# Optimization experiments

Measured on AMD Instinct MI355X. Metric: run time of the kernel, lower is better.

The kernel has to match this reference:

```python
import jax, jax.numpy as jnp
import numpy as np

T_MAX = 20  # max_seq_length


def setup_inputs() -> dict:
    key = jax.random.key(0)
    ks = jax.random.split(key, 24)
    B, H, A, V, Tc = 64, 512, 512, 50257, 19
    s = 0.02
    inp = {}
    inp["features"] = jax.random.normal(ks[0], (B, H), jnp.float32)
    inp["captions"] = jax.random.randint(ks[1], (B, Tc), 0, V)
    lens = jax.random.randint(ks[2], (B, 1), 1, T_MAX + 1)
    inp["lengths"] = -jnp.sort(-lens, axis=0)  # descending so sort_ind is identity
    inp["embed_table"] = jax.random.uniform(ks[3], (V, H), jnp.float32, -0.1, 0.1)
    # LSTM cell (PyTorch layout): input = [emb; attended] -> 2H
    inp["W_ih"] = jax.random.normal(ks[4], (4 * H, 2 * H), jnp.float32) * s
    inp["W_hh"] = jax.random.normal(ks[5], (4 * H, H), jnp.float32) * s
    inp["b_ih"] = jnp.zeros((4 * H,), jnp.float32)
    inp["b_hh"] = jnp.zeros((4 * H,), jnp.float32)
    # attention
    inp["W_enc"] = jax.random.normal(ks[6], (H, A), jnp.float32) * s
    inp["b_enc"] = jnp.zeros((A,), jnp.float32)
    inp["W_dec"] = jax.random.normal(ks[7], (H, A), jnp.float32) * s
    inp["b_dec"] = jnp.zeros((A,), jnp.float32)
    inp["W_full"] = jax.random.normal(ks[8], (A, 1), jnp.float32) * s
    inp["b_full"] = jnp.zeros((1,), jnp.float32)
    # init_h / init_c / f_beta / fc
    inp["W_hinit"] = jax.random.normal(ks[9], (H, H), jnp.float32) * s
    inp["b_hinit"] = jnp.zeros((H,), jnp.float32)
    inp["W_cinit"] = jax.random.normal(ks[10], (H, H), jnp.float32) * s
    inp["b_cinit"] = jnp.zeros((H,), jnp.float32)
    inp["W_beta"] = jax.random.normal(ks[11], (H, H), jnp.float32) * s
    inp["b_beta"] = jnp.zeros((H,), jnp.float32)
    inp["W_fc"] = jax.random.uniform(ks[12], (H, V), jnp.float32, -0.1, 0.1)
    inp["b_fc"] = jnp.zeros((V,), jnp.float32)
    return inp


def _decode(features, embed_table, W_ih, W_hh, b_ih, b_hh, W_enc, b_enc,
            W_dec, b_dec, W_full, b_full, W_hinit, b_hinit, W_cinit, b_cinit,
            W_beta, b_beta, W_fc, b_fc, captions, lengths):
    B, H = features.shape
    emb = embed_table[captions]                               # (B, T-1, H)
    embeddings = jnp.concatenate([features[:, None, :], emb], axis=1)  # (B, T, H)
    encoder_out = features[:, None, :]                        # (B, 1, H) num_pixels=1
    mean_enc = encoder_out.mean(axis=1)
    h0 = mean_enc @ W_hinit + b_hinit
    c0 = mean_enc @ W_cinit + b_cinit
    att1 = encoder_out @ W_enc + b_enc                        # (B, 1, A), time-invariant
    lens = lengths[:, 0]

    def step(carry, xs):
        h, c = carry
        emb_t, t = xs
        # attention
        att2 = h @ W_dec + b_dec                              # (B, A)
        e = jax.nn.relu(att1 + att2[:, None, :]) @ W_full + b_full  # (B, 1, 1)
        alpha = jax.nn.softmax(e[..., 0], axis=1)             # (B, 1)
        awe = (encoder_out * alpha[..., None]).sum(axis=1)    # (B, H)
        gate = jax.nn.sigmoid(h @ W_beta + b_beta)
        awe = gate * awe
        # LSTM cell (PyTorch gate order i, f, g, o)
        x = jnp.concatenate([emb_t, awe], axis=1)             # (B, 2H)
        gates = x @ W_ih.T + b_ih + h @ W_hh.T + b_hh
        i, f, g, o = jnp.split(gates, 4, axis=1)
        c_new = jax.nn.sigmoid(f) * c + jax.nn.sigmoid(i) * jnp.tanh(g)
        h_new = jax.nn.sigmoid(o) * jnp.tanh(c_new)
        preds = h_new @ W_fc + b_fc                           # (B, V)
        mask = (t < lens)[:, None]
        h = jnp.where(mask, h_new, h)
        c = jnp.where(mask, c_new, c)
        out_t = jnp.where(mask, preds, jnp.zeros_like(preds))
        return (h, c), out_t

    xs = (embeddings.transpose(1, 0, 2), jnp.arange(T_MAX))
    _, outs = jax.lax.scan(step, (h0, c0), xs)                # (T, B, V)
    return outs.transpose(1, 0, 2)                            # (B, T, V)


def reference(features, captions, lengths, embed_table, W_ih, W_hh, b_ih, b_hh,
              W_enc, b_enc, W_dec, b_dec, W_full, b_full, W_hinit, b_hinit,
              W_cinit, b_cinit, W_beta, b_beta, W_fc, b_fc):
    return _decode(features, embed_table, W_ih, W_hh, b_ih, b_hh, W_enc, b_enc,
                   W_dec, b_dec, W_full, b_full, W_hinit, b_hinit, W_cinit,
                   b_cinit, W_beta, b_beta, W_fc, b_fc, captions, lengths)
```

## Files before the change

kernel.cpp:

```cpp
#include <hip/hip_runtime.h>
#include <hip/hip_bf16.h>


#define VV 50257
#define VP 50304
#define TT 20
#define NWRK 32
#define NTILES 6288

typedef __attribute__((ext_vector_type(4))) float f32x4;
typedef __attribute__((ext_vector_type(8))) short bf16x8;

#define MFMA(a,b,c) __builtin_amdgcn_mfma_f32_16x16x32_bf16((a),(b),(c),0,0,0)

__device__ __forceinline__ unsigned short f2bf(float f){
  union { float f; unsigned int u; } v; v.f = f;
  unsigned int u = v.u;
  return (unsigned short)((u + 0x7FFFu + ((u >> 16) & 1u)) >> 16);
}
__device__ __forceinline__ float sigf(float x){ return 1.f/(1.f + expf(-x)); }

__device__ __forceinline__ void gload_lds16(const unsigned short* g, unsigned short* l){
  __builtin_amdgcn_global_load_lds(
      (const __attribute__((address_space(1))) unsigned int*)g,
      (__attribute__((address_space(3))) unsigned int*)l, 16, 0, 0);
}

__device__ __forceinline__ void co_load16(bf16x8* d, const unsigned short* p){
  asm volatile("global_load_dwordx4 %0, %1, off sc0 sc1" : "=v"(*d) : "v"(p));
}
__device__ __forceinline__ void co_store2(unsigned short* p, unsigned short v){
  asm volatile("global_store_short %0, %1, off sc0 sc1" :: "v"(p), "v"(v) : "memory");
}
__device__ __forceinline__ unsigned int co_load_u32(const unsigned int* p){
  unsigned int r;
  asm volatile("global_load_dword %0, %1, off sc0 sc1\n\ts_waitcnt vmcnt(0)"
               : "=v"(r) : "v"(p) : "memory");
  return r;
}

__device__ __forceinline__ void gbar(unsigned int* cnt, unsigned int target){
  asm volatile("s_waitcnt vmcnt(0)" ::: "memory");
  __syncthreads();
  if(threadIdx.x == 0){
    atomicAdd(cnt, 1u);
    while(co_load_u32(cnt) < target) __builtin_amdgcn_s_sleep(1);
  }
  __syncthreads();
}


__global__ __launch_bounds__(256) void cvt_weights(const float* __restrict__ Wih,
    const float* __restrict__ Whh, unsigned short* __restrict__ Wcomb,
    unsigned short* __restrict__ We){
  int j = blockIdx.x; int tid = threadIdx.x;
  for(int q=0;q<4;q++){ int k = tid + 256*q;
    float v = (k < 512) ? Whh[j*512 + k] : Wih[j*1024 + k];
    Wcomb[(size_t)j*1024 + k] = f2bf(v); }
  for(int q=0;q<2;q++){ int k = tid + 256*q;
    We[(size_t)j*512 + k] = f2bf(Wih[j*1024 + k]); }
}

__global__ __launch_bounds__(256) void transpose_cvt(const float* __restrict__ src,
    unsigned short* __restrict__ dst, int R, int C){
  __shared__ float tile[64][65];
  int c0 = blockIdx.x*64, r0 = blockIdx.y*64;
  int tx = threadIdx.x & 63, ty = threadIdx.x >> 6;
  for(int i=0;i<16;i++){
    int r = ty + i*4; int sc = c0 + tx;
    tile[r][tx] = (sc < C) ? src[(size_t)(r0+r)*C + sc] : 0.f;
  }
  __syncthreads();
  for(int i=0;i<16;i++){
    int cl = ty + i*4;
    dst[(size_t)(c0+cl)*R + r0 + tx] = f2bf(tile[tx][cl]);
  }
}

__global__ __launch_bounds__(128) void build_emb(const float* __restrict__ feat,
    const float* __restrict__ emb, const int* __restrict__ cap,
    unsigned short* __restrict__ EmbMat){
  int m = blockIdx.x; int t = m >> 6, b = m & 63;
  const float* src = (t == 0) ? (feat + b*512) : (emb + (size_t)cap[b*19 + (t-1)]*512);
  for(int q=0;q<4;q++){ int k = threadIdx.x + 128*q;
    EmbMat[(size_t)m*512 + k] = f2bf(src[k]); }
}

__global__ __launch_bounds__(512) void init_hc(const float* __restrict__ feat,
    const float* __restrict__ Whi, const float* __restrict__ bhi,
    const float* __restrict__ Wci, const float* __restrict__ bci,
    unsigned short* __restrict__ x0, float* __restrict__ c){
  int j = threadIdx.x; int b0 = blockIdx.x*4;
  float ah[4], ac[4];
#pragma unroll
  for(int r=0;r<4;r++){ ah[r] = bhi[j]; ac[r] = bci[j]; }
  for(int k=0;k<512;k++){
    float wh = Whi[k*512 + j], wc = Wci[k*512 + j];
#pragma unroll
    for(int r=0;r<4;r++){
      float f = feat[(b0+r)*512 + k];
      ah[r] += f*wh; ac[r] += f*wc;
    }
  }
#pragma unroll
  for(int r=0;r<4;r++){
    x0[(b0+r)*512 + j] = f2bf(ah[r]);
    c[(b0+r)*512 + j] = ac[r];
  }
}

template<int EPIL>
__global__ __launch_bounds__(256) void gemm2(const unsigned short* __restrict__ Abf,
    const unsigned short* __restrict__ Bbf, const float* __restrict__ bias1,
    const float* __restrict__ bias2, const int* __restrict__ lensp,
    float* __restrict__ Cout, int MT){
  __shared__ __align__(16) char smem[32768];
  unsigned short* As = (unsigned short*)smem;
  unsigned short* Bs = (unsigned short*)(smem + 16384);
  float* et = (float*)smem;

  const int nwg = gridDim.x;
  const int id = blockIdx.x;
  const int q = nwg >> 3, rr = nwg & 7;
  const int xcd = id & 7, pos = id >> 3;
  const int work = (xcd < rr) ? (xcd*(q+1) + pos) : (rr*(q+1) + (xcd-rr)*q + pos);
  const int m0 = (work % MT) * 128;
  const int n0 = (work / MT) * 128;
  const int tid = threadIdx.x, lane = tid & 63, w = tid >> 6;
  const int wr = w >> 1, wc = w & 1;
  const int lrow = lane >> 3, lcol = (lane & 7) * 8;
  const int l15 = lane & 15, lhi = lane >> 4;

  f32x4 acc[4][4];
#pragma unroll
  for(int i=0;i<4;i++)
#pragma unroll
    for(int j=0;j<4;j++) acc[i][j] = f32x4{0.f,0.f,0.f,0.f};

  for(int k0=0;k0<512;k0+=64){
    __syncthreads();
#pragma unroll
    for(int i=0;i<4;i++){
      int c = w*4 + i;
      int row = c*8 + lrow;
      gload_lds16(Abf + (size_t)(m0+row)*512 + k0 + lcol, As + c*512);
      gload_lds16(Bbf + (size_t)(n0+row)*512 + k0 + lcol, Bs + c*512);
    }
    asm volatile("s_waitcnt vmcnt(0)" ::: "memory");
    __syncthreads();
#pragma unroll
    for(int kk=0;kk<64;kk+=32){
      bf16x8 af[4], bfv[4];
#pragma unroll
      for(int mf=0;mf<4;mf++)
        af[mf] = *(const bf16x8*)(As + (wr*64 + mf*16 + l15)*64 + kk + lhi*8);
#pragma unroll
      for(int nf=0;nf<4;nf++)
        bfv[nf] = *(const bf16x8*)(Bs + (wc*64 + nf*16 + l15)*64 + kk + lhi*8);
#pragma unroll
      for(int mf=0;mf<4;mf++)
#pragma unroll
        for(int nf=0;nf<4;nf++)
          acc[mf][nf] = MFMA(af[mf], bfv[nf], acc[mf][nf]);
    }
  }

  if constexpr (EPIL == 0){
#pragma unroll
    for(int mf=0;mf<4;mf++)
#pragma unroll
      for(int nf=0;nf<4;nf++){
        int n = n0 + wc*64 + nf*16 + l15;
#pragma unroll
        for(int r=0;r<4;r++){
          int m = m0 + wr*64 + mf*16 + lhi*4 + r;
          int gate = n >> 9, col = n & 511;
          Cout[((size_t)m*512 + col)*4 + gate] = acc[mf][nf][r] + bias1[n] + bias2[n];
        }
      }
  } else {
    const bool edge = (n0 + 128 > VV);
    for(int half=0; half<2; half++){
      __syncthreads();
      if(wr == half){
#pragma unroll
        for(int mf=0;mf<4;mf++)
#pragma unroll
          for(int nf=0;nf<4;nf++){
            int n = n0 + wc*64 + nf*16 + l15;
#pragma unroll
            for(int r=0;r<4;r++){
              int m = m0 + half*64 + mf*16 + lhi*4 + r;
              int b = m/20, tt = m%20;
              float v = (tt < lensp[b]) ? (acc[mf][nf][r] + bias1[n]) : 0.f;
              et[(mf*16 + lhi*4 + r)*128 + wc*64 + nf*16 + l15] = v;
            }
          }
      }
      __syncthreads();
#pragma unroll
      for(int qq=0;qq<8;qq++){
        int idx = tid + 256*qq;
        int row = idx >> 5, c4 = idx & 31;
        int m = m0 + half*64 + row;
        const float* er = et + row*128;
        if(!edge){
          size_t bdw = (size_t)m*VV + n0;
          int al = (int)((4 - (bdw & 3)) & 3);
          int chunks = (128 - al) >> 2;
          int tail = (128 - al) & 3;
          if(c4 < chunks){
            int s0 = al + c4*4;
            f32x4 v; v[0]=er[s0]; v[1]=er[s0+1]; v[2]=er[s0+2]; v[3]=er[s0+3];
            *(f32x4*)(Cout + bdw + s0) = v;
          }
          if(c4 < al) Cout[bdw + c4] = er[c4];
          if(c4 < tail){ int s1 = al + chunks*4 + c4; Cout[bdw + s1] = er[s1]; }
        } else {
#pragma unroll
          for(int i=0;i<4;i++){
            int cg = n0 + c4*4 + i;
            if(cg < VV) Cout[(size_t)m*VV + cg] = er[c4*4 + i];
          }
        }
      }
    }
  }
}

__global__ __launch_bounds__(256) void recur(
    const unsigned short* __restrict__ Wcomb,
    const unsigned short* __restrict__ Wbt,
    const float* __restrict__ bbeta,
    const float* __restrict__ feat,
    const float* __restrict__ E4,
    const float* __restrict__ c0,
    const int* __restrict__ lens,
    unsigned short* xbuf,
    unsigned short* awbuf,
    unsigned short* __restrict__ hs,
    unsigned int* ctrs,
    const float* __restrict__ Wfc, unsigned short* __restrict__ Wfct){
  extern __shared__ char LDS[];
  char* WCb = LDS;
  char* WBb = LDS + 131072;
  char* STb = LDS + 147456;
  int* lsh = (int*)LDS;
  const int tid = threadIdx.x;

  if(tid == 0){
    unsigned xcc = 99;
    asm volatile("s_getreg_b32 %0, hwreg(HW_REG_XCC_ID)" : "=s"(xcc));
    unsigned my = 0xffffffffu;
    if(xcc == 0) my = atomicAdd(&ctrs[0], 1u);
    lsh[0] = (my < NWRK) ? 1 : 0;
    lsh[1] = (int)my;
  }
  __syncthreads();
  const int iswork = lsh[0];
  const int widx = lsh[1];
  __syncthreads();

  if(!iswork){
    float (*tile)[65] = (float(*)[65])LDS;
    int tx = tid & 63, ty = tid >> 6;
    for(;;){
      __syncthreads();
      if(tid == 0) lsh[0] = (int)atomicAdd(&ctrs[16], 1u);
      __syncthreads();
      int tb = lsh[0];
      __syncthreads();
      if(tb >= NTILES) return;
      int c0t = (tb % 786)*64, r0 = (tb / 786)*64;
      for(int i=0;i<16;i++){
        int r = ty + i*4; int sc = c0t + tx;
        tile[r][tx] = (sc < VV) ? Wfc[(size_t)(r0+r)*VV + sc] : 0.f;
      }
      __syncthreads();
      for(int i=0;i<16;i++){
        int cl = ty + i*4;
        Wfct[(size_t)(c0t+cl)*512 + r0 + tx] = f2bf(tile[tx][cl]);
      }
    }
  }

  const int lane = tid & 63, w = tid >> 6;
  const int l15 = lane & 15, lhi = lane >> 4;
  const int jj0 = widx * 16;
  const int jj = jj0 + l15;
  const int arow = w*16 + l15;
  unsigned int* barcnt = &ctrs[32];

  for(int cid = tid; cid < 8192; cid += 256){
    int gr = cid >> 7, cc = cid & 127;
    size_t g = (size_t)(gr >> 4)*512 + jj0 + (gr & 15);
    bf16x8 v = *(const bf16x8*)(Wcomb + g*1024 + cc*8);
    *(bf16x8*)(WCb + gr*2048 + ((cc*16) ^ ((gr & 7) << 4))) = v;
  }
  for(int cid = tid; cid < 1024; cid += 256){
    int r = cid >> 6, cc = cid & 63;
    bf16x8 v = *(const bf16x8*)(Wbt + (size_t)(jj0 + r)*512 + cc*8);
    *(bf16x8*)(WBb + r*1024 + ((cc*16) ^ ((r & 7) << 4))) = v;
  }

  float c_reg[4], fe[4]; int ln[4];
#pragma unroll
  for(int r=0;r<4;r++){
    int b = w*16 + lhi*4 + r;
    c_reg[r] = c0[b*512 + jj];
    fe[r]    = feat[b*512 + jj];
    ln[r]    = lens[b];
  }
  const float bb = bbeta[jj];
  const int kc_h = widx >> 3;
  __syncthreads();

  for(int t=0;t<TT;t++){
    f32x4 acca = f32x4{0.f,0.f,0.f,0.f};
    f32x4 accg[4];
#pragma unroll
    for(int i=0;i<4;i++) accg[i] = f32x4{0.f,0.f,0.f,0.f};
    unsigned short hold[4];

    for(int kc=0; kc<4; kc++){
      __syncthreads();
      bf16x8 sv[4];
#pragma unroll
      for(int qq=0;qq<4;qq++){
        int cid = tid + 256*qq; int row = cid >> 4, cc = cid & 15;
        co_load16(&sv[qq], xbuf + row*512 + kc*128 + cc*8);
      }
      asm volatile("s_waitcnt vmcnt(0)" ::: "memory");
      __builtin_amdgcn_sched_barrier(0);
#pragma unroll
      for(int qq=0;qq<4;qq++){
        int cid = tid + 256*qq; int row = cid >> 4, cc = cid & 15;
        *(bf16x8*)(STb + row*256 + ((cc*16) ^ ((row & 7) << 4))) = sv[qq];
      }
      __syncthreads();
      if(kc == kc_h){
#pragma unroll
        for(int r=0;r<4;r++){
          int b = w*16 + lhi*4 + r;
          int cl2 = 2*(jj & 127);
          hold[r] = *(const unsigned short*)(STb + b*256 + (cl2 ^ ((b & 7) << 4)));
        }
      }
#pragma unroll
      for(int ks=0; ks<4; ks++){
        int kl2 = ks*64 + lhi*16;
        int kg2 = kc*256 + kl2;
        bf16x8 a = *(const bf16x8*)(STb + arow*256 + (kl2 ^ ((arow & 7) << 4)));
        bf16x8 wb = *(const bf16x8*)(WBb + l15*1024 + (kg2 ^ ((l15 & 7) << 4)));
        acca = MFMA(a, wb, acca);
#pragma unroll
        for(int nf=0; nf<4; nf++){
          int gr = nf*16 + l15;
          bf16x8 wg = *(const bf16x8*)(WCb + gr*2048 + (kg2 ^ ((gr & 7) << 4)));
          accg[nf] = MFMA(a, wg, accg[nf]);
        }
      }
    }
#pragma unroll
    for(int r=0;r<4;r++){
      int b = w*16 + lhi*4 + r;
      float g = sigf(acca[r] + bb);
      co_store2(awbuf + b*512 + jj, f2bf(g * fe[r]));
    }
    gbar(barcnt, (unsigned)(2*t+1)*NWRK);

    f32x4 e4v[4];
#pragma unroll
    for(int r=0;r<4;r++){
      int b = w*16 + lhi*4 + r;
      e4v[r] = *(const f32x4*)(E4 + (((size_t)(t*64 + b))*512 + jj)*4);
    }

    for(int kc=0; kc<4; kc++){
      __syncthreads();
      bf16x8 sv[4];
#pragma unroll
      for(int qq=0;qq<4;qq++){
        int cid = tid + 256*qq; int row = cid >> 4, cc = cid & 15;
        co_load16(&sv[qq], awbuf + row*512 + kc*128 + cc*8);
      }
      asm volatile("s_waitcnt vmcnt(0)" ::: "memory");
      __builtin_amdgcn_sched_barrier(0);
#pragma unroll
      for(int qq=0;qq<4;qq++){
        int cid = tid + 256*qq; int row = cid >> 4, cc = cid & 15;
        *(bf16x8*)(STb + row*256 + ((cc*16) ^ ((row & 7) << 4))) = sv[qq];
      }
      __syncthreads();
#pragma unroll
      for(int ks=0; ks<4; ks++){
        int kl2 = ks*64 + lhi*16;
        int kg2 = 1024 + kc*256 + kl2;
        bf16x8 a = *(const bf16x8*)(STb + arow*256 + (kl2 ^ ((arow & 7) << 4)));
#pragma unroll
        for(int nf=0; nf<4; nf++){
          int gr = nf*16 + l15;
          bf16x8 wg = *(const bf16x8*)(WCb + gr*2048 + (kg2 ^ ((gr & 7) << 4)));
          accg[nf] = MFMA(a, wg, accg[nf]);
        }
      }
    }

#pragma unroll
    for(int r=0;r<4;r++){
      int b = w*16 + lhi*4 + r;
      float iv = sigf(accg[0][r] + e4v[r][0]);
      float fv = sigf(accg[1][r] + e4v[r][1]);
      float gv = tanhf(accg[2][r] + e4v[r][2]);
      float ov = sigf(accg[3][r] + e4v[r][3]);
      float cn = fv*c_reg[r] + iv*gv;
      float hn = ov * tanhf(cn);
      bool valid = t < ln[r];
      if(valid) c_reg[r] = cn;
      unsigned short hb = valid ? f2bf(hn) : hold[r];
      hs[((size_t)(b*20 + t))*512 + jj] = hb;
      co_store2(xbuf + b*512 + jj, hb);
    }
    if(t < TT-1) gbar(barcnt, (unsigned)(2*t+2)*NWRK);
  }
}

extern "C" void kernel_launch(void* const* d_in, const int* in_sizes, int n_in,
                              void* d_out, int out_size, void* d_ws, size_t ws_size,
                              hipStream_t stream){
  const float* feat  = (const float*)d_in[0];
  const int*   cap   = (const int*)  d_in[1];
  const int*   lens  = (const int*)  d_in[2];
  const float* emb   = (const float*)d_in[3];
  const float* Wih   = (const float*)d_in[4];
  const float* Whh   = (const float*)d_in[5];
  const float* bih   = (const float*)d_in[6];
  const float* bhh   = (const float*)d_in[7];
  const float* Whi   = (const float*)d_in[14];
  const float* bhi   = (const float*)d_in[15];
  const float* Wci   = (const float*)d_in[16];
  const float* bci   = (const float*)d_in[17];
  const float* Wbeta = (const float*)d_in[18];
  const float* bbeta = (const float*)d_in[19];
  const float* Wfc   = (const float*)d_in[20];
  const float* bfc   = (const float*)d_in[21];
  float* out = (float*)d_out;

  char* ws = (char*)d_ws;
  size_t off = 0;
  auto alloc = [&](size_t bytes)->void*{
    void* p = ws + off; off += (bytes + 1023) & ~(size_t)1023; return p; };
  unsigned short* Wcomb  = (unsigned short*)alloc((size_t)2048*1024*2);
  unsigned short* We     = (unsigned short*)alloc((size_t)2048*512*2);
  unsigned short* Wbt    = (unsigned short*)alloc((size_t)512*512*2);
  unsigned short* Wfct   = (unsigned short*)alloc((size_t)VP*512*2);
  unsigned short* EmbMat = (unsigned short*)alloc((size_t)1280*512*2);
  float*          E4     = (float*)alloc((size_t)1280*2048*4);
  unsigned short* xbuf   = (unsigned short*)alloc((size_t)64*512*2);
  unsigned short* awbuf  = (unsigned short*)alloc((size_t)64*512*2);
  float*          cbuf   = (float*)alloc((size_t)64*512*4);
  unsigned short* hs     = (unsigned short*)alloc((size_t)1280*512*2);
  unsigned int*   ctrs   = (unsigned int*)alloc(256);

  static_cast<void>(hipFuncSetAttribute((const void*)recur,
      hipFuncAttributeMaxDynamicSharedMemorySize, 163840));

  hipMemsetAsync(ctrs, 0, 256, stream);
  cvt_weights<<<2048, 256, 0, stream>>>(Wih, Whh, Wcomb, We);
  transpose_cvt<<<dim3(8,8), 256, 0, stream>>>(Wbeta, Wbt, 512, 512);
  build_emb<<<1280, 128, 0, stream>>>(feat, emb, cap, EmbMat);
  init_hc<<<16, 512, 0, stream>>>(feat, Whi, bhi, Wci, bci, xbuf, cbuf);

  gemm2<0><<<160, 256, 0, stream>>>(EmbMat, We, bih, bhh, nullptr, E4, 10);

  recur<<<2080, 256, 163840, stream>>>(Wcomb, Wbt, bbeta, feat, E4, cbuf, lens,
                                       xbuf, awbuf, hs, ctrs, Wfc, Wfct);

  gemm2<1><<<3930, 256, 0, stream>>>(hs, Wfct, bfc, nullptr, lens, out, 10);
}
```

Baseline: 613.6 us.

## Replace atomic grid barrier with per-block flags and load operands directly to registers

```diff
diff --git a/kernel.cpp b/kernel.cpp
--- a/kernel.cpp
+++ b/kernel.cpp
@@ -26,86 +26,80 @@
       (__attribute__((address_space(3))) unsigned int*)l, 16, 0, 0);
 }
 
-__device__ __forceinline__ void co_load16(bf16x8* d, const unsigned short* p){
-  asm volatile("global_load_dwordx4 %0, %1, off sc0 sc1" : "=v"(*d) : "v"(p));
-}
-__device__ __forceinline__ void co_store2(unsigned short* p, unsigned short v){
-  asm volatile("global_store_short %0, %1, off sc0 sc1" :: "v"(p), "v"(v) : "memory");
-}
-__device__ __forceinline__ unsigned int co_load_u32(const unsigned int* p){
-  unsigned int r;
-  asm volatile("global_load_dword %0, %1, off sc0 sc1\n\ts_waitcnt vmcnt(0)"
-               : "=v"(r) : "v"(p) : "memory");
-  return r;
-}
-
-__device__ __forceinline__ void gbar(unsigned int* cnt, unsigned int target){
+__device__ __forceinline__ void l2_load16(bf16x8* d, const unsigned short* p){
+  asm volatile("global_load_dwordx4 %0, %1, off sc0" : "=v"(*d) : "v"(p));
+}
+__device__ __forceinline__ void l2_store2(unsigned short* p, unsigned short v){
+  asm volatile("global_store_short %0, %1, off sc0" :: "v"(p), "v"(v) : "memory");
+}
+
+__device__ __forceinline__ void gbar(unsigned int* flags, int widx, unsigned target){
   asm volatile("s_waitcnt vmcnt(0)" ::: "memory");
   __syncthreads();
   if(threadIdx.x == 0){
-    atomicAdd(cnt, 1u);
-    while(co_load_u32(cnt) < target) __builtin_amdgcn_s_sleep(1);
+    asm volatile("global_store_dword %0, %1, off sc0 sc1"
+                 :: "v"(flags + widx), "v"(target) : "memory");
+  }
+  if(threadIdx.x < 64){
+    const unsigned int* p = flags + (threadIdx.x & 31);
+    for(;;){
+      unsigned v;
+      asm volatile("global_load_dword %0, %1, off sc0 sc1\n\ts_waitcnt vmcnt(0)"
+                   : "=v"(v) : "v"(p) : "memory");
+      if(__all((int)(v >= target))) break;
+      __builtin_amdgcn_s_sleep(1);
+    }
   }
   __syncthreads();
 }
 
-
-__global__ __launch_bounds__(256) void cvt_weights(const float* __restrict__ Wih,
+__global__ __launch_bounds__(256) void prep(const float* __restrict__ Wih,
     const float* __restrict__ Whh, unsigned short* __restrict__ Wcomb,
-    unsigned short* __restrict__ We){
-  int j = blockIdx.x; int tid = threadIdx.x;
-  for(int q=0;q<4;q++){ int k = tid + 256*q;
-    float v = (k < 512) ? Whh[j*512 + k] : Wih[j*1024 + k];
-    Wcomb[(size_t)j*1024 + k] = f2bf(v); }
-  for(int q=0;q<2;q++){ int k = tid + 256*q;
-    We[(size_t)j*512 + k] = f2bf(Wih[j*1024 + k]); }
-}
-
-__global__ __launch_bounds__(256) void transpose_cvt(const float* __restrict__ src,
-    unsigned short* __restrict__ dst, int R, int C){
-  __shared__ float tile[64][65];
-  int c0 = blockIdx.x*64, r0 = blockIdx.y*64;
-  int tx = threadIdx.x & 63, ty = threadIdx.x >> 6;
-  for(int i=0;i<16;i++){
-    int r = ty + i*4; int sc = c0 + tx;
-    tile[r][tx] = (sc < C) ? src[(size_t)(r0+r)*C + sc] : 0.f;
-  }
-  __syncthreads();
-  for(int i=0;i<16;i++){
-    int cl = ty + i*4;
-    dst[(size_t)(c0+cl)*R + r0 + tx] = f2bf(tile[tx][cl]);
-  }
-}
-
-__global__ __launch_bounds__(128) void build_emb(const float* __restrict__ feat,
-    const float* __restrict__ emb, const int* __restrict__ cap,
-    unsigned short* __restrict__ EmbMat){
-  int m = blockIdx.x; int t = m >> 6, b = m & 63;
-  const float* src = (t == 0) ? (feat + b*512) : (emb + (size_t)cap[b*19 + (t-1)]*512);
-  for(int q=0;q<4;q++){ int k = threadIdx.x + 128*q;
-    EmbMat[(size_t)m*512 + k] = f2bf(src[k]); }
-}
-
-__global__ __launch_bounds__(512) void init_hc(const float* __restrict__ feat,
+    unsigned short* __restrict__ We,
+    const float* __restrict__ Wbeta, unsigned short* __restrict__ Wbt,
+    const float* __restrict__ feat, const float* __restrict__ emb,
+    const int* __restrict__ cap, unsigned short* __restrict__ EmbMat,
     const float* __restrict__ Whi, const float* __restrict__ bhi,
     const float* __restrict__ Wci, const float* __restrict__ bci,
-    unsigned short* __restrict__ x0, float* __restrict__ c){
-  int j = threadIdx.x; int b0 = blockIdx.x*4;
-  float ah[4], ac[4];
-#pragma unroll
-  for(int r=0;r<4;r++){ ah[r] = bhi[j]; ac[r] = bci[j]; }
-  for(int k=0;k<512;k++){
-    float wh = Whi[k*512 + j], wc = Wci[k*512 + j];
-#pragma unroll
-    for(int r=0;r<4;r++){
-      float f = feat[(b0+r)*512 + k];
-      ah[r] += f*wh; ac[r] += f*wc;
-    }
-  }
-#pragma unroll
-  for(int r=0;r<4;r++){
-    x0[(b0+r)*512 + j] = f2bf(ah[r]);
-    c[(b0+r)*512 + j] = ac[r];
+    unsigned short* __restrict__ xbuf, float* __restrict__ cbuf){
+  __shared__ float tile[64][65];
+  const int blk = blockIdx.x, tid = threadIdx.x;
+  if(blk < 2048){
+    int j = blk;
+    for(int q=0;q<4;q++){ int k = tid + 256*q;
+      float v = (k < 512) ? Whh[j*512 + k] : Wih[j*1024 + k];
+      Wcomb[(size_t)j*1024 + k] = f2bf(v); }
+    for(int q=0;q<2;q++){ int k = tid + 256*q;
+      We[(size_t)j*512 + k] = f2bf(Wih[j*1024 + k]); }
+  } else if(blk < 2112){
+    int tb = blk - 2048;
+    int c0 = (tb & 7)*64, r0 = (tb >> 3)*64;
+    int tx = tid & 63, ty = tid >> 6;
+    for(int i=0;i<16;i++){
+      int r = ty + i*4;
+      tile[r][tx] = Wbeta[(size_t)(r0+r)*512 + c0 + tx];
+    }
+    __syncthreads();
+    for(int i=0;i<16;i++){
+      int cl = ty + i*4;
+      Wbt[(size_t)(c0+cl)*512 + r0 + tx] = f2bf(tile[tx][cl]);
+    }
+  } else if(blk < 3392){
+    int m = blk - 2112; int t = m >> 6, b = m & 63;
+    const float* src = (t == 0) ? (feat + b*512) : (emb + (size_t)cap[b*19 + (t-1)]*512);
+    for(int q=0;q<2;q++){ int k = tid + 256*q;
+      EmbMat[(size_t)m*512 + k] = f2bf(src[k]); }
+  } else {
+    int b = blk - 3392;
+    float ah0 = bhi[tid], ah1 = bhi[tid+256];
+    float ac0 = bci[tid], ac1 = bci[tid+256];
+    for(int k=0;k<512;k++){
+      float f = feat[b*512 + k];
+      ah0 += f * Whi[k*512 + tid];     ah1 += f * Whi[k*512 + tid + 256];
+      ac0 += f * Wci[k*512 + tid];     ac1 += f * Wci[k*512 + tid + 256];
+    }
+    xbuf[b*512 + tid] = f2bf(ah0);  xbuf[b*512 + tid + 256] = f2bf(ah1);
+    cbuf[b*512 + tid] = ac0;        cbuf[b*512 + tid + 256] = ac1;
   }
 }
 
@@ -244,7 +238,6 @@
   extern __shared__ char LDS[];
   char* WCb = LDS;
   char* WBb = LDS + 131072;
-  char* STb = LDS + 147456;
   int* lsh = (int*)LDS;
   const int tid = threadIdx.x;
 
@@ -289,7 +282,7 @@
   const int jj0 = widx * 16;
   const int jj = jj0 + l15;
   const int arow = w*16 + l15;
-  unsigned int* barcnt = &ctrs[32];
+  unsigned int* flags = &ctrs[32];
 
   for(int cid = tid; cid < 8192; cid += 256){
     int gr = cid >> 7, cc = cid & 127;
@@ -303,71 +296,50 @@
     *(bf16x8*)(WBb + r*1024 + ((cc*16) ^ ((r & 7) << 4))) = v;
   }
 
-  float c_reg[4], fe[4]; int ln[4];
+  float c_reg[4], fe[4]; int ln[4]; unsigned short hold[4];
 #pragma unroll
   for(int r=0;r<4;r++){
     int b = w*16 + lhi*4 + r;
     c_reg[r] = c0[b*512 + jj];
     fe[r]    = feat[b*512 + jj];
     ln[r]    = lens[b];
+    hold[r]  = xbuf[b*512 + jj];
   }
   const float bb = bbeta[jj];
-  const int kc_h = widx >> 3;
+  const unsigned short* pAx = xbuf  + (size_t)arow*512 + lhi*8;
+  const unsigned short* pAw = awbuf + (size_t)arow*512 + lhi*8;
   __syncthreads();
 
   for(int t=0;t<TT;t++){
+    bf16x8 a[16];
+#pragma unroll
+    for(int i=0;i<16;i++) l2_load16(&a[i], pAx + i*32);
+    asm volatile("s_waitcnt vmcnt(0)" ::: "memory");
+    __builtin_amdgcn_sched_barrier(0);
+
     f32x4 acca = f32x4{0.f,0.f,0.f,0.f};
     f32x4 accg[4];
 #pragma unroll
     for(int i=0;i<4;i++) accg[i] = f32x4{0.f,0.f,0.f,0.f};
-    unsigned short hold[4];
-
-    for(int kc=0; kc<4; kc++){
-      __syncthreads();
-      bf16x8 sv[4];
-#pragma unroll
-      for(int qq=0;qq<4;qq++){
-        int cid = tid + 256*qq; int row = cid >> 4, cc = cid & 15;
-        co_load16(&sv[qq], xbuf + row*512 + kc*128 + cc*8);
-      }
-      asm volatile("s_waitcnt vmcnt(0)" ::: "memory");
-      __builtin_amdgcn_sched_barrier(0);
-#pragma unroll
-      for(int qq=0;qq<4;qq++){
-        int cid = tid + 256*qq; int row = cid >> 4, cc = cid & 15;
-        *(bf16x8*)(STb + row*256 + ((cc*16) ^ ((row & 7) << 4))) = sv[qq];
-      }
-      __syncthreads();
-      if(kc == kc_h){
-#pragma unroll
-        for(int r=0;r<4;r++){
-          int b = w*16 + lhi*4 + r;
-          int cl2 = 2*(jj & 127);
-          hold[r] = *(const unsigned short*)(STb + b*256 + (cl2 ^ ((b & 7) << 4)));
-        }
-      }
-#pragma unroll
-      for(int ks=0; ks<4; ks++){
-        int kl2 = ks*64 + lhi*16;
-        int kg2 = kc*256 + kl2;
-        bf16x8 a = *(const bf16x8*)(STb + arow*256 + (kl2 ^ ((arow & 7) << 4)));
-        bf16x8 wb = *(const bf16x8*)(WBb + l15*1024 + (kg2 ^ ((l15 & 7) << 4)));
-        acca = MFMA(a, wb, acca);
-#pragma unroll
-        for(int nf=0; nf<4; nf++){
-          int gr = nf*16 + l15;
-          bf16x8 wg = *(const bf16x8*)(WCb + gr*2048 + (kg2 ^ ((gr & 7) << 4)));
-          accg[nf] = MFMA(a, wg, accg[nf]);
-        }
+#pragma unroll
+    for(int i=0;i<16;i++){
+      int kb2 = i*64 + lhi*16;
+      bf16x8 wb = *(const bf16x8*)(WBb + l15*1024 + (kb2 ^ ((l15 & 7) << 4)));
+      acca = MFMA(a[i], wb, acca);
+#pragma unroll
+      for(int nf=0; nf<4; nf++){
+        int gr = nf*16 + l15;
+        bf16x8 wg = *(const bf16x8*)(WCb + gr*2048 + (kb2 ^ ((gr & 7) << 4)));
+        accg[nf] = MFMA(a[i], wg, accg[nf]);
       }
     }
 #pragma unroll
     for(int r=0;r<4;r++){
       int b = w*16 + lhi*4 + r;
       float g = sigf(acca[r] + bb);
-      co_store2(awbuf + b*512 + jj, f2bf(g * fe[r]));
-    }
-    gbar(barcnt, (unsigned)(2*t+1)*NWRK);
+      l2_store2(awbuf + b*512 + jj, f2bf(g * fe[r]));
+    }
+    gbar(flags, widx, (unsigned)(2*t+1));
 
     f32x4 e4v[4];
 #pragma unroll
@@ -375,34 +347,18 @@
       int b = w*16 + lhi*4 + r;
       e4v[r] = *(const f32x4*)(E4 + (((size_t)(t*64 + b))*512 + jj)*4);
     }
-
-    for(int kc=0; kc<4; kc++){
-      __syncthreads();
-      bf16x8 sv[4];
-#pragma unroll
-      for(int qq=0;qq<4;qq++){
-        int cid = tid + 256*qq; int row = cid >> 4, cc = cid & 15;
-        co_load16(&sv[qq], awbuf + row*512 + kc*128 + cc*8);
-      }
-      asm volatile("s_waitcnt vmcnt(0)" ::: "memory");
-      __builtin_amdgcn_sched_barrier(0);
-#pragma unroll
-      for(int qq=0;qq<4;qq++){
-        int cid = tid + 256*qq; int row = cid >> 4, cc = cid & 15;
-        *(bf16x8*)(STb + row*256 + ((cc*16) ^ ((row & 7) << 4))) = sv[qq];
-      }
-      __syncthreads();
-#pragma unroll
-      for(int ks=0; ks<4; ks++){
-        int kl2 = ks*64 + lhi*16;
-        int kg2 = 1024 + kc*256 + kl2;
-        bf16x8 a = *(const bf16x8*)(STb + arow*256 + (kl2 ^ ((arow & 7) << 4)));
-#pragma unroll
-        for(int nf=0; nf<4; nf++){
-          int gr = nf*16 + l15;
-          bf16x8 wg = *(const bf16x8*)(WCb + gr*2048 + (kg2 ^ ((gr & 7) << 4)));
-          accg[nf] = MFMA(a, wg, accg[nf]);
-        }
+#pragma unroll
+    for(int i=0;i<16;i++) l2_load16(&a[i], pAw + i*32);
+    asm volatile("s_waitcnt vmcnt(0)" ::: "memory");
+    __builtin_amdgcn_sched_barrier(0);
+#pragma unroll
+    for(int i=0;i<16;i++){
+      int kb2 = 1024 + i*64 + lhi*16;
+#pragma unroll
+      for(int nf=0; nf<4; nf++){
+        int gr = nf*16 + l15;
+        bf16x8 wg = *(const bf16x8*)(WCb + gr*2048 + (kb2 ^ ((gr & 7) << 4)));
+        accg[nf] = MFMA(a[i], wg, accg[nf]);
       }
     }
 
@@ -418,10 +374,11 @@
       bool valid = t < ln[r];
       if(valid) c_reg[r] = cn;
       unsigned short hb = valid ? f2bf(hn) : hold[r];
+      hold[r] = hb;
       hs[((size_t)(b*20 + t))*512 + jj] = hb;
-      co_store2(xbuf + b*512 + jj, hb);
-    }
-    if(t < TT-1) gbar(barcnt, (unsigned)(2*t+2)*NWRK);
+      l2_store2(xbuf + b*512 + jj, hb);
+    }
+    if(t < TT-1) gbar(flags, widx, (unsigned)(2*t+2));
   }
 }
 
@@ -463,17 +420,16 @@
   unsigned int*   ctrs   = (unsigned int*)alloc(256);
 
   static_cast<void>(hipFuncSetAttribute((const void*)recur,
-      hipFuncAttributeMaxDynamicSharedMemorySize, 163840));
+      hipFuncAttributeMaxDynamicSharedMemorySize, 147456));
 
   hipMemsetAsync(ctrs, 0, 256, stream);
-  cvt_weights<<<2048, 256, 0, stream>>>(Wih, Whh, Wcomb, We);
-  transpose_cvt<<<dim3(8,8), 256, 0, stream>>>(Wbeta, Wbt, 512, 512);
-  build_emb<<<1280, 128, 0, stream>>>(feat, emb, cap, EmbMat);
-  init_hc<<<16, 512, 0, stream>>>(feat, Whi, bhi, Wci, bci, xbuf, cbuf);
+
+  prep<<<3456, 256, 0, stream>>>(Wih, Whh, Wcomb, We, Wbeta, Wbt, feat, emb,
+                                 cap, EmbMat, Whi, bhi, Wci, bci, xbuf, cbuf);
 
   gemm2<0><<<160, 256, 0, stream>>>(EmbMat, We, bih, bhh, nullptr, E4, 10);
 
-  recur<<<2080, 256, 163840, stream>>>(Wcomb, Wbt, bbeta, feat, E4, cbuf, lens,
+  recur<<<2080, 256, 147456, stream>>>(Wcomb, Wbt, bbeta, feat, E4, cbuf, lens,
                                        xbuf, awbuf, hs, ctrs, Wfc, Wfct);
 
   gemm2<1><<<3930, 256, 0, stream>>>(hs, Wfct, bfc, nullptr, lens, out, 10);
```

Measured after the change: 598.3 us. 2.5% less time.
